# Kernel tuning notes

Measured on AMD Instinct MI355X. Metric: run time of the kernel, lower is better.

Reference implementation:

```python
import jax, jax.numpy as jnp
import numpy as np

N_SOTU, N_TAXON = 100000, 20000
E, EL = 800000, 200000
D_S, D_T, H = 256, 128, 256


def setup_inputs() -> dict:
    key = jax.random.key(0)
    ks = jax.random.split(key, 32)
    nrm = lambda k, shp: jax.random.normal(k, shp, jnp.float32) * 0.05
    inp = {}
    inp["x_sotu"] = nrm(ks[0], (N_SOTU, D_S))
    inp["x_taxon"] = nrm(ks[1], (N_TAXON, D_T))
    inp["edge_src"] = jax.random.randint(ks[2], (E,), 0, N_SOTU)   # sotu end
    inp["edge_dst"] = jax.random.randint(ks[3], (E,), 0, N_TAXON)  # taxon end
    inp["label_src"] = jax.random.randint(ks[4], (EL,), 0, N_SOTU)
    inp["label_dst"] = jax.random.randint(ks[5], (EL,), 0, N_TAXON)
    # conv1, edge type sotu->taxon
    inp["Wl1_st"] = nrm(ks[6], (H, D_S)); inp["bl1_st"] = jnp.zeros((H,), jnp.float32)
    inp["Wr1_st"] = nrm(ks[7], (H, D_T))
    # conv1, edge type taxon->sotu (reverse)
    inp["Wl1_ts"] = nrm(ks[8], (H, D_T)); inp["bl1_ts"] = jnp.zeros((H,), jnp.float32)
    inp["Wr1_ts"] = nrm(ks[9], (H, D_S))
    # conv2 (hidden -> hidden) per edge type
    inp["Wl2_st"] = nrm(ks[10], (H, H)); inp["bl2_st"] = jnp.zeros((H,), jnp.float32)
    inp["Wr2_st"] = nrm(ks[11], (H, H))
    inp["Wl2_ts"] = nrm(ks[12], (H, H)); inp["bl2_ts"] = jnp.zeros((H,), jnp.float32)
    inp["Wr2_ts"] = nrm(ks[13], (H, H))
    # final per-node-type linear (to_hetero duplicates Linear per node type)
    inp["Wlin_s"] = nrm(ks[14], (H, H)); inp["blin_s"] = jnp.zeros((H,), jnp.float32)
    inp["Wlin_t"] = nrm(ks[15], (H, H)); inp["blin_t"] = jnp.zeros((H,), jnp.float32)
    # edge decoder MLP
    inp["Wd1"] = nrm(ks[16], (H, 2 * H)); inp["bd1"] = jnp.zeros((H,), jnp.float32)
    inp["Wd2"] = nrm(ks[17], (1, H));     inp["bd2"] = jnp.zeros((1,), jnp.float32)
    return inp


def _sage(x_src, x_dst, src, dst, Wl, bl, Wr):
    """PyG SAGEConv (mean aggr): lin_l(mean of neighbor src feats) + lin_r(x_dst)."""
    n_dst = x_dst.shape[0]
    msum = jax.ops.segment_sum(x_src[src], dst, num_segments=n_dst)
    cnt = jax.ops.segment_sum(jnp.ones(src.shape, x_src.dtype), dst, num_segments=n_dst)
    m = msum / jnp.maximum(cnt, 1.0)[:, None]
    return m @ Wl.T + bl + x_dst @ Wr.T


def reference(x_sotu, x_taxon, edge_src, edge_dst, label_src, label_dst,
              Wl1_st, bl1_st, Wr1_st, Wl1_ts, bl1_ts, Wr1_ts,
              Wl2_st, bl2_st, Wr2_st, Wl2_ts, bl2_ts, Wr2_ts,
              Wlin_s, blin_s, Wlin_t, blin_t, Wd1, bd1, Wd2, bd2):
    # layer 1 (hetero SAGE, aggr='sum' over single incoming edge type per node type)
    h1_t = jax.nn.relu(_sage(x_sotu, x_taxon, edge_src, edge_dst, Wl1_st, bl1_st, Wr1_st))
    h1_s = jax.nn.relu(_sage(x_taxon, x_sotu, edge_dst, edge_src, Wl1_ts, bl1_ts, Wr1_ts))
    # layer 2
    h2_t = jax.nn.relu(_sage(h1_s, h1_t, edge_src, edge_dst, Wl2_st, bl2_st, Wr2_st))
    h2_s = jax.nn.relu(_sage(h1_t, h1_s, edge_dst, edge_src, Wl2_ts, bl2_ts, Wr2_ts))
    # per-node-type output projection
    z_s = h2_s @ Wlin_s.T + blin_s
    z_t = h2_t @ Wlin_t.T + blin_t
    # edge decoder: gather endpoint embeddings, concat, 2-layer MLP
    z = jnp.concatenate([z_s[label_src], z_t[label_dst]], axis=-1)  # [EL, 2H]
    h = jax.nn.relu(z @ Wd1.T + bd1)
    return (h @ Wd2.T + bd2).reshape(-1)  # [EL]
```

## Files before the change

### kernel.cpp

```cpp
#include <hip/hip_runtime.h>


constexpr int NS = 100000, NT = 20000;
constexpr int E_EDGES = 800000, EL_EDGES = 200000;
constexpr int DS = 256, DT = 128, H = 256;

constexpr int NB_T = 79, SH_T = 8, VB_T = 17;
constexpr int NB_S = 98, SH_S = 10, VB_S = 15;
constexpr int BIN_CAP = 96, CHUNK = 2048;
constexpr int CVT_BLOCKS = 2048;

typedef __attribute__((ext_vector_type(8))) short short8;
typedef __attribute__((ext_vector_type(4))) float float4v;
typedef __attribute__((ext_vector_type(8))) _Float16 half8v;
typedef unsigned short ushort_t;

__device__ __forceinline__ float bf2f(unsigned int u) {
    union { unsigned int i; float f; } x; x.i = u << 16; return x.f;
}
__device__ __forceinline__ unsigned short f2bf(float f) {
    union { float f; unsigned int i; } x; x.f = f;
    unsigned int r = x.i + 0x7FFFu + ((x.i >> 16) & 1u);
    return (unsigned short)(r >> 16);
}


struct GemmJob {
    const ushort_t* A1; const ushort_t* W1; int K1;
    const ushort_t* A2; const ushort_t* W2; int K2;
    const ushort_t* Add; const float* bias;
    void* C; int M; int flags;
};

struct GatherJob {
    const ushort_t* X; const int* rowptr; const int* cnt; const int* col;
    ushort_t* out; int N;
};

__device__ __forceinline__ void gemm_body(const GemmJob& jb, int bid)
{
    __shared__ ushort_t As[128][40];
    __shared__ ushort_t Bs[128][40];
    const int tid = threadIdx.x;
    const int M = jb.M;

    const int nx = (M + 127) >> 7;
    const int nx8 = nx & ~7;
    int rowblk, colblk;
    if (bid < nx8 * 2) {
        const int group = bid >> 4;
        const int xcd = bid & 7;
        const int half = (bid >> 3) & 1;
        rowblk = group * 8 + xcd;
        colblk = half;
    } else {
        const int r = bid - nx8 * 2;
        rowblk = nx8 + (r >> 1);
        colblk = r & 1;
    }
    const int row0 = rowblk * 128, col0 = colblk * 128;

    const int wave = tid >> 6, lane = tid & 63;
    const int wrow = (wave >> 1) * 32;
    const int wcol = (wave & 1) * 64;
    const int m16 = lane & 15, quad = lane >> 4;
    const int sr = tid >> 2;
    const int skc = (tid & 3) * 8;

    float4v acc[2][4];
#pragma unroll
    for (int i = 0; i < 2; i++)
#pragma unroll
        for (int j = 0; j < 4; j++) acc[i][j] = (float4v){0.f, 0.f, 0.f, 0.f};

#pragma unroll 1
    for (int pass = 0; pass < 2; pass++) {
        const ushort_t* A = pass ? jb.A2 : jb.A1;
        const ushort_t* W = pass ? jb.W2 : jb.W1;
        const int K = pass ? jb.K2 : jb.K1;
        if (!A) break;
        const int gra = row0 + sr;
        const bool oka = gra < M;
        const ushort_t* Ap = A + (size_t)gra * K + skc;
        const ushort_t* Wp = W + (size_t)(col0 + sr) * K + skc;

        uint4 a0 = make_uint4(0, 0, 0, 0);
        if (oka) a0 = *(const uint4*)Ap;
        uint4 b0 = *(const uint4*)Wp;

        for (int k0 = 0; k0 < K; k0 += 32) {
            __syncthreads();
            *(uint4*)&As[sr][skc] = a0;
            *(uint4*)&Bs[sr][skc] = b0;
            __syncthreads();
            if (k0 + 32 < K) {
                a0 = make_uint4(0, 0, 0, 0);
                if (oka) a0 = *(const uint4*)(Ap + k0 + 32);
                b0 = *(const uint4*)(Wp + k0 + 32);
            }
            short8 af[2], bf[4];
#pragma unroll
            for (int i = 0; i < 2; i++)
                af[i] = *(const short8*)&As[wrow + i * 16 + m16][quad * 8];
#pragma unroll
            for (int j = 0; j < 4; j++)
                bf[j] = *(const short8*)&Bs[wcol + j * 16 + m16][quad * 8];
#pragma unroll
            for (int i = 0; i < 2; i++)
#pragma unroll
                for (int j = 0; j < 4; j++)
                    acc[i][j] = __builtin_amdgcn_mfma_f32_16x16x32_bf16(
                        af[i], bf[j], acc[i][j], 0, 0, 0);
        }
    }

    const bool relu = jb.flags & 1, f16out = jb.flags & 2;
#pragma unroll
    for (int i = 0; i < 2; i++) {
        const int rbase = row0 + wrow + i * 16 + quad * 4;
#pragma unroll
        for (int r = 0; r < 4; r++) {
            const int row = rbase + r;
            if (row >= M) continue;
#pragma unroll
            for (int j = 0; j < 4; j++) {
                const int col = col0 + wcol + j * 16 + m16;
                float v = acc[i][j][r];
                if (jb.Add) v += bf2f((unsigned int)jb.Add[(size_t)row * 256 + col]);
                if (jb.bias) v += jb.bias[col];
                if (relu) v = fmaxf(v, 0.f);
                if (f16out) ((_Float16*)jb.C)[(size_t)row * 256 + col] = (_Float16)v;
                else ((ushort_t*)jb.C)[(size_t)row * 256 + col] = f2bf(v);
            }
        }
    }
}

__device__ __forceinline__ void gather_body(const GatherJob& g, int gb)
{
    const int node = gb * 16 + (threadIdx.x >> 5);
    const int c = (threadIdx.x & 31) * 8;
    if (node >= g.N) return;
    const int beg = g.rowptr[node];
    const int deg = g.cnt[node];
    const int end = beg + deg;
    const ushort_t* __restrict__ X = g.X;
    const int* __restrict__ col = g.col;
    float a[8] = {0, 0, 0, 0, 0, 0, 0, 0};
    float b[8] = {0, 0, 0, 0, 0, 0, 0, 0};
    int i = beg;
    for (; i + 1 < end; i += 2) {
        uint4 v = *(const uint4*)&X[(size_t)col[i] * 256 + c];
        uint4 w = *(const uint4*)&X[(size_t)col[i + 1] * 256 + c];
        a[0] += bf2f(v.x & 0xffff); a[1] += bf2f(v.x >> 16);
        a[2] += bf2f(v.y & 0xffff); a[3] += bf2f(v.y >> 16);
        a[4] += bf2f(v.z & 0xffff); a[5] += bf2f(v.z >> 16);
        a[6] += bf2f(v.w & 0xffff); a[7] += bf2f(v.w >> 16);
        b[0] += bf2f(w.x & 0xffff); b[1] += bf2f(w.x >> 16);
        b[2] += bf2f(w.y & 0xffff); b[3] += bf2f(w.y >> 16);
        b[4] += bf2f(w.z & 0xffff); b[5] += bf2f(w.z >> 16);
        b[6] += bf2f(w.w & 0xffff); b[7] += bf2f(w.w >> 16);
    }
    if (i < end) {
        uint4 v = *(const uint4*)&X[(size_t)col[i] * 256 + c];
        a[0] += bf2f(v.x & 0xffff); a[1] += bf2f(v.x >> 16);
        a[2] += bf2f(v.y & 0xffff); a[3] += bf2f(v.y >> 16);
        a[4] += bf2f(v.z & 0xffff); a[5] += bf2f(v.z >> 16);
        a[6] += bf2f(v.w & 0xffff); a[7] += bf2f(v.w >> 16);
    }
    float inv = 1.f / fmaxf((float)deg, 1.f);
    uint4 o;
    o.x = (unsigned int)f2bf((a[0] + b[0]) * inv) | ((unsigned int)f2bf((a[1] + b[1]) * inv) << 16);
    o.y = (unsigned int)f2bf((a[2] + b[2]) * inv) | ((unsigned int)f2bf((a[3] + b[3]) * inv) << 16);
    o.z = (unsigned int)f2bf((a[4] + b[4]) * inv) | ((unsigned int)f2bf((a[5] + b[5]) * inv) << 16);
    o.w = (unsigned int)f2bf((a[6] + b[6]) * inv) | ((unsigned int)f2bf((a[7] + b[7]) * inv) << 16);
    *(uint4*)&g.out[(size_t)node * 256 + c] = o;
}

__global__ __launch_bounds__(512) void mgemm_kernel(GemmJob a)
{
    gemm_body(a, blockIdx.x);
}

__global__ __launch_bounds__(512) void gemm_gather_kernel(GemmJob a, int ablocks,
                                                          GatherJob g)
{
    const int bid = blockIdx.x;
    if (bid < ablocks) gemm_body(a, bid);
    else gather_body(g, bid - ablocks);
}

__global__ __launch_bounds__(512) void gemm_gemm_kernel(GemmJob a, int ablocks,
                                                        GemmJob b)
{
    const int bid = blockIdx.x;
    if (bid < ablocks) gemm_body(a, bid);
    else gemm_body(b, bid - ablocks);
}

struct CvtJobs {
    const float* src[14];
    ushort_t* dst[14];
    int n4[14];
    int cnt;
};

__global__ __launch_bounds__(256) void cvt_kernel(CvtJobs jb, int nchunks)
{
    const int t = threadIdx.x;
#pragma unroll 1
    for (int ch = blockIdx.x; ch < nchunks; ch += gridDim.x) {
        int idx = ch << 10;
        int k = 0;
        while (idx >= jb.n4[k]) { idx -= jb.n4[k]; ++k; }
        const float4* __restrict__ s = (const float4*)jb.src[k];
        ushort_t* __restrict__ d = jb.dst[k];
        const int base = idx + t;
        float4 v0 = s[base];
        float4 v1 = s[base + 256];
        float4 v2 = s[base + 512];
        float4 v3 = s[base + 768];
        uint2 o0, o1, o2, o3;
        o0.x = (unsigned int)f2bf(v0.x) | ((unsigned int)f2bf(v0.y) << 16);
        o0.y = (unsigned int)f2bf(v0.z) | ((unsigned int)f2bf(v0.w) << 16);
        o1.x = (unsigned int)f2bf(v1.x) | ((unsigned int)f2bf(v1.y) << 16);
        o1.y = (unsigned int)f2bf(v1.z) | ((unsigned int)f2bf(v1.w) << 16);
        o2.x = (unsigned int)f2bf(v2.x) | ((unsigned int)f2bf(v2.y) << 16);
        o2.y = (unsigned int)f2bf(v2.z) | ((unsigned int)f2bf(v2.w) << 16);
        o3.x = (unsigned int)f2bf(v3.x) | ((unsigned int)f2bf(v3.y) << 16);
        o3.y = (unsigned int)f2bf(v3.z) | ((unsigned int)f2bf(v3.w) << 16);
        *(uint2*)(d + (size_t)base * 4) = o0;
        *(uint2*)(d + (size_t)(base + 256) * 4) = o1;
        *(uint2*)(d + (size_t)(base + 512) * 4) = o2;
        *(uint2*)(d + (size_t)(base + 768) * 4) = o3;
    }
}

__global__ __launch_bounds__(256) void count_kernel(
    const int* __restrict__ src, const int* __restrict__ dst,
    int* __restrict__ cnt_s, int* __restrict__ cnt_t, int E)
{
    const int base = blockIdx.x * 1024 + threadIdx.x;
    const int e0 = base, e1 = base + 256, e2 = base + 512, e3 = base + 768;
    int s0 = 0, s1 = 0, s2 = 0, s3 = 0;
    int d0 = 0, d1 = 0, d2 = 0, d3 = 0;
    if (e0 < E) { s0 = src[e0]; d0 = dst[e0]; }
    if (e1 < E) { s1 = src[e1]; d1 = dst[e1]; }
    if (e2 < E) { s2 = src[e2]; d2 = dst[e2]; }
    if (e3 < E) { s3 = src[e3]; d3 = dst[e3]; }
    if (e0 < E) { atomicAdd(&cnt_s[s0], 1); atomicAdd(&cnt_t[d0], 1); }
    if (e1 < E) { atomicAdd(&cnt_s[s1], 1); atomicAdd(&cnt_t[d1], 1); }
    if (e2 < E) { atomicAdd(&cnt_s[s2], 1); atomicAdd(&cnt_t[d2], 1); }
    if (e3 < E) { atomicAdd(&cnt_s[s3], 1); atomicAdd(&cnt_t[d3], 1); }
}

__global__ __launch_bounds__(256) void fold_kernel(
    const float* __restrict__ Wd1, const float* __restrict__ bd1,
    const float* __restrict__ Wlin_s, const float* __restrict__ blin_s,
    const float* __restrict__ Wlin_t, const float* __restrict__ blin_t,
    float* __restrict__ Wc_s, float* __restrict__ Wc_t,
    float* __restrict__ bu, float* __restrict__ bv)
{
    const int b = blockIdx.x, t = threadIdx.x;
    if (b < 256) {
        float s = 0.f;
        for (int k = 0; k < 256; k++) s += Wd1[b * 512 + k] * Wlin_s[k * 256 + t];
        Wc_s[b * 256 + t] = s;
    } else if (b < 512) {
        const int h = b - 256;
        float s = 0.f;
        for (int k = 0; k < 256; k++) s += Wd1[h * 512 + 256 + k] * Wlin_t[k * 256 + t];
        Wc_t[h * 256 + t] = s;
    } else {
        float su = 0.f, sv = 0.f;
        for (int k = 0; k < 256; k++) {
            su += Wd1[t * 512 + k] * blin_s[k];
            sv += Wd1[t * 512 + 256 + k] * blin_t[k];
        }
        bu[t] = bd1[t] + su;
        bv[t] = sv;
    }
}

__global__ __launch_bounds__(256) void psum_kernel(
    const int* __restrict__ cnt_s, const int* __restrict__ cnt_t,
    int* __restrict__ bsum_s, int* __restrict__ bsum_t, int nbS)
{
    const bool isS = (int)blockIdx.x < nbS;
    const int blk = isS ? blockIdx.x : blockIdx.x - nbS;
    const int N = isS ? NS : NT;
    const int* cnt = isS ? cnt_s : cnt_t;
    int* bsum = isS ? bsum_s : bsum_t;
    __shared__ int sdata[256];
    const int t = threadIdx.x;
    const int base = blk * 1024;
    int s = 0;
    for (int i = t; i < 1024; i += 256) {
        int idx = base + i;
        s += (idx < N) ? cnt[idx] : 0;
    }
    sdata[t] = s; __syncthreads();
    for (int off = 128; off > 0; off >>= 1) {
        if (t < off) sdata[t] += sdata[t + off];
        __syncthreads();
    }
    if (t == 0) bsum[blk] = sdata[0];
}

__global__ void sbsum_kernel(int* __restrict__ bsum_s, int* __restrict__ bsum_t,
                             int nbS, int nbT)
{
    if (threadIdx.x != 0) return;
    int* b = blockIdx.x ? bsum_t : bsum_s;
    int nb = blockIdx.x ? nbT : nbS;
    int run = 0;
    for (int i = 0; i < nb; i++) { int v = b[i]; b[i] = run; run += v; }
}

__global__ __launch_bounds__(256) void sblock_kernel(
    const int* __restrict__ cnt_s, const int* __restrict__ cnt_t,
    const int* __restrict__ bsum_s, const int* __restrict__ bsum_t,
    int* __restrict__ rowptr_s, int* __restrict__ rowptr_t, int nbS)
{
    const bool isS = (int)blockIdx.x < nbS;
    const int blk = isS ? blockIdx.x : blockIdx.x - nbS;
    const int N = isS ? NS : NT;
    const int* cnt = isS ? cnt_s : cnt_t;
    const int* bsum = isS ? bsum_s : bsum_t;
    int* rowptr = isS ? rowptr_s : rowptr_t;
    __shared__ int sc[256];
    const int t = threadIdx.x;
    const int base = blk * 1024 + t * 4;
    int v[4]; int s = 0;
#pragma unroll
    for (int j = 0; j < 4; j++) {
        int idx = base + j;
        v[j] = (idx < N) ? cnt[idx] : 0;
        s += v[j];
    }
    sc[t] = s; __syncthreads();
    for (int off = 1; off < 256; off <<= 1) {
        int add = (t >= off) ? sc[t - off] : 0;
        __syncthreads();
        sc[t] += add;
        __syncthreads();
    }
    int excl = sc[t] - s + bsum[blk];
#pragma unroll
    for (int j = 0; j < 4; j++) {
        int idx = base + j;
        if (idx < N) rowptr[idx] = excl;
        if (idx == N - 1) rowptr[N] = excl + v[j];
        excl += v[j];
    }
}

__global__ void binit_kernel(const int* __restrict__ rowptr_t,
                             const int* __restrict__ rowptr_s,
                             int* __restrict__ gcur_t, int* __restrict__ gcur_s)
{
    int t = threadIdx.x;
    if (t < NB_T) gcur_t[t] = rowptr_t[t << SH_T];
    if (t < NB_S) gcur_s[t] = rowptr_s[t << SH_S];
}

__global__ __launch_bounds__(256) void binA_kernel(
    const int* __restrict__ key, const int* __restrict__ val, int E,
    int nbins, int shift, int vbits,
    int* __restrict__ gcur, unsigned* __restrict__ stg)
{
    __shared__ unsigned bins[NB_S * BIN_CAP];
    __shared__ int lcnt[NB_S], gbase[NB_S];
    const int tid = threadIdx.x;
    const int base = blockIdx.x * CHUNK;
    for (int i = tid; i < nbins; i += 256) lcnt[i] = 0;
    __syncthreads();
    const unsigned lowmask = (1u << shift) - 1u;
#pragma unroll
    for (int k = 0; k < CHUNK / 256; k++) {
        int e = base + k * 256 + tid;
        if (e < E) {
            int kk = key[e];
            int b = kk >> shift;
            unsigned pk = (((unsigned)kk & lowmask) << vbits) | (unsigned)val[e];
            int c = atomicAdd(&lcnt[b], 1);
            if (c < BIN_CAP) bins[b * BIN_CAP + c] = pk;
            else { int p = atomicAdd(&gcur[b], 1); stg[p] = pk; }
        }
    }
    __syncthreads();
    if (tid < nbins) gbase[tid] = atomicAdd(&gcur[tid], min(lcnt[tid], BIN_CAP));
    __syncthreads();
    for (int b = 0; b < nbins; b++) {
        int c = min(lcnt[b], BIN_CAP);
        for (int i = tid; i < c; i += 256) stg[gbase[b] + i] = bins[b * BIN_CAP + i];
    }
}

__global__ __launch_bounds__(256) void binB_kernel(
    const unsigned* __restrict__ stg, const int* __restrict__ rowptr,
    int N, int node_per, int vbits, int* __restrict__ colout)
{
    __shared__ int cur[1024];
    const int tid = threadIdx.x;
    const int node0 = blockIdx.x * node_per;
    const int nn = min(node_per, N - node0);
    for (int i = tid; i < nn; i += 256) cur[i] = rowptr[node0 + i];
    const int estart = rowptr[node0];
    const int eend = rowptr[node0 + nn];
    __syncthreads();
    const unsigned vmask = (1u << vbits) - 1u;
    for (int i = estart + tid; i < eend; i += 256) {
        unsigned v = stg[i];
        int kl = (int)(v >> vbits);
        int pos = atomicAdd(&cur[kl], 1);
        colout[pos] = (int)(v & vmask);
    }
}

__global__ __launch_bounds__(256) void edge_score_kernel(
    const _Float16* __restrict__ U, const _Float16* __restrict__ V,
    const int* __restrict__ ls, const int* __restrict__ ld,
    const float* __restrict__ Wd2, const float* __restrict__ bd2,
    float* __restrict__ out, int EL)
{
    const int l32 = threadIdx.x & 31;
    const int e = blockIdx.x * 8 + (threadIdx.x >> 5);
    if (e >= EL) return;
    const int c = l32 * 8;
    half8v u = *(const half8v*)&U[(size_t)ls[e] * 256 + c];
    half8v v = *(const half8v*)&V[(size_t)ld[e] * 256 + c];
    float4 w0 = *(const float4*)&Wd2[c];
    float4 w1 = *(const float4*)&Wd2[c + 4];
    float s = fmaxf((float)u[0] + (float)v[0], 0.f) * w0.x
            + fmaxf((float)u[1] + (float)v[1], 0.f) * w0.y
            + fmaxf((float)u[2] + (float)v[2], 0.f) * w0.z
            + fmaxf((float)u[3] + (float)v[3], 0.f) * w0.w
            + fmaxf((float)u[4] + (float)v[4], 0.f) * w1.x
            + fmaxf((float)u[5] + (float)v[5], 0.f) * w1.y
            + fmaxf((float)u[6] + (float)v[6], 0.f) * w1.z
            + fmaxf((float)u[7] + (float)v[7], 0.f) * w1.w;
#pragma unroll
    for (int m = 16; m >= 1; m >>= 1) s += __shfl_xor(s, m, 64);
    if (l32 == 0) out[e] = s + bd2[0];
}

extern "C" void kernel_launch(void* const* d_in, const int* in_sizes, int n_in,
                              void* d_out, int out_size, void* d_ws, size_t ws_size,
                              hipStream_t stream)
{
    const float* x_sotu  = (const float*)d_in[0];
    const float* x_taxon = (const float*)d_in[1];
    const int* edge_src  = (const int*)d_in[2];
    const int* edge_dst  = (const int*)d_in[3];
    const int* label_src = (const int*)d_in[4];
    const int* label_dst = (const int*)d_in[5];
    const float* Wl1_st = (const float*)d_in[6];
    const float* bl1_st = (const float*)d_in[7];
    const float* Wr1_st = (const float*)d_in[8];
    const float* Wl1_ts = (const float*)d_in[9];
    const float* bl1_ts = (const float*)d_in[10];
    const float* Wr1_ts = (const float*)d_in[11];
    const float* Wl2_st = (const float*)d_in[12];
    const float* bl2_st = (const float*)d_in[13];
    const float* Wr2_st = (const float*)d_in[14];
    const float* Wl2_ts = (const float*)d_in[15];
    const float* bl2_ts = (const float*)d_in[16];
    const float* Wr2_ts = (const float*)d_in[17];
    const float* Wlin_s = (const float*)d_in[18];
    const float* blin_s = (const float*)d_in[19];
    const float* Wlin_t = (const float*)d_in[20];
    const float* blin_t = (const float*)d_in[21];
    const float* Wd1 = (const float*)d_in[22];
    const float* bd1 = (const float*)d_in[23];
    const float* Wd2 = (const float*)d_in[24];
    const float* bd2 = (const float*)d_in[25];

    int* wi = (int*)d_ws;
    size_t io = 0;
    int* cnt_s   = wi + io; io += NS;
    int* cnt_t   = wi + io; io += NT;
    int* rowptr_s = wi + io; io += NS + 8;
    int* rowptr_t = wi + io; io += NT + 8;
    int* col_s   = wi + io; io += E_EDGES;
    int* col_t   = wi + io; io += E_EDGES;
    unsigned* stg_s = (unsigned*)(wi + io); io += E_EDGES;
    unsigned* stg_t = (unsigned*)(wi + io); io += E_EDGES;
    int* bsum_s  = wi + io; io += 128;
    int* bsum_t  = wi + io; io += 128;
    int* gcur_t  = wi + io; io += 128;
    int* gcur_s  = wi + io; io += 128;
    io = (io + 63) & ~(size_t)63;

    ushort_t* wb = (ushort_t*)(wi + io);
    size_t bo = 0;
    ushort_t* m_s  = wb + bo; bo += (size_t)NS * H;
    ushort_t* h1_s = wb + bo; bo += (size_t)NS * H;
    ushort_t* m_t  = wb + bo; bo += (size_t)NT * H;
    ushort_t* h1_t = wb + bo; bo += (size_t)NT * H;
    ushort_t* h2_s = wb + bo; bo += (size_t)NS * H;
    ushort_t* h2_t = wb + bo; bo += (size_t)NT * H;
    ushort_t* xs_b = wb + bo; bo += (size_t)NS * DS;
    ushort_t* xt_b = wb + bo; bo += (size_t)NT * DT;
    ushort_t* Pt   = wb + bo; bo += (size_t)NT * H;
    ushort_t* wb_l1st = wb + bo; bo += H * DS;
    ushort_t* wb_r1st = wb + bo; bo += H * DT;
    ushort_t* wb_l1ts = wb + bo; bo += H * DT;
    ushort_t* wb_r1ts = wb + bo; bo += H * DS;
    ushort_t* wb_l2st = wb + bo; bo += H * H;
    ushort_t* wb_r2st = wb + bo; bo += H * H;
    ushort_t* wb_l2ts = wb + bo; bo += H * H;
    ushort_t* wb_r2ts = wb + bo; bo += H * H;
    ushort_t* wcb_s   = wb + bo; bo += H * H;
    ushort_t* wcb_t   = wb + bo; bo += H * H;
    bo = (bo + 7) & ~(size_t)7;

    float* wf = (float*)(wb + bo);
    size_t fo = 0;
    float* Wc_s = wf + fo; fo += H * H;
    float* Wc_t = wf + fo; fo += H * H;
    float* bu   = wf + fo; fo += 256;
    float* bv   = wf + fo; fo += 256;

    _Float16* U = (_Float16*)m_s;
    _Float16* V = (_Float16*)m_t;

    const dim3 blk(256);
    const dim3 blk512(512);
    auto mgn = [](int M) { return ((M + 127) / 128) * 2; };
    auto ggn = [](int N) { return (N + 15) / 16; };
    const int nbS = (NS + 1023) / 1024;
    const int nbT = (NT + 1023) / 1024;
    const int nA = (E_EDGES + CHUNK - 1) / CHUNK;

    fold_kernel<<<513, blk, 0, stream>>>(Wd1, bd1, Wlin_s, blin_s, Wlin_t, blin_t,
                                         Wc_s, Wc_t, bu, bv);

    hipMemsetAsync(cnt_s, 0, (size_t)(NS + NT) * sizeof(int), stream);
    count_kernel<<<(E_EDGES + 1023) / 1024, blk, 0, stream>>>(
        edge_src, edge_dst, cnt_s, cnt_t, E_EDGES);

    {
        CvtJobs jb; int c = 0, total4 = 0;
        auto addj = [&](const float* s, ushort_t* d, int n) {
            jb.src[c] = s; jb.dst[c] = d; jb.n4[c] = n / 4; total4 += n / 4; c++;
        };
        addj(x_sotu, xs_b, NS * DS);
        addj(x_taxon, xt_b, NT * DT);
        addj(Wl1_st, wb_l1st, H * DS);
        addj(Wr1_st, wb_r1st, H * DT);
        addj(Wl1_ts, wb_l1ts, H * DT);
        addj(Wr1_ts, wb_r1ts, H * DS);
        addj(Wl2_st, wb_l2st, H * H);
        addj(Wr2_st, wb_r2st, H * H);
        addj(Wl2_ts, wb_l2ts, H * H);
        addj(Wr2_ts, wb_r2ts, H * H);
        addj(Wc_s, wcb_s, H * H);
        addj(Wc_t, wcb_t, H * H);
        jb.cnt = c;
        const int nchunks = total4 >> 10;
        const int cvb = nchunks < CVT_BLOCKS ? nchunks : CVT_BLOCKS;
        cvt_kernel<<<cvb, blk, 0, stream>>>(jb, nchunks);
    }

    psum_kernel<<<nbS + nbT, blk, 0, stream>>>(cnt_s, cnt_t, bsum_s, bsum_t, nbS);
    sbsum_kernel<<<2, 64, 0, stream>>>(bsum_s, bsum_t, nbS, nbT);
    sblock_kernel<<<nbS + nbT, blk, 0, stream>>>(cnt_s, cnt_t, bsum_s, bsum_t,
                                                 rowptr_s, rowptr_t, nbS);
    binit_kernel<<<1, blk, 0, stream>>>(rowptr_t, rowptr_s, gcur_t, gcur_s);
    binA_kernel<<<nA, blk, 0, stream>>>(edge_dst, edge_src, E_EDGES,
                                        NB_T, SH_T, VB_T, gcur_t, stg_t);
    binA_kernel<<<nA, blk, 0, stream>>>(edge_src, edge_dst, E_EDGES,
                                        NB_S, SH_S, VB_S, gcur_s, stg_s);
    binB_kernel<<<NB_T, blk, 0, stream>>>(stg_t, rowptr_t, NT, 1 << SH_T, VB_T, col_t);
    binB_kernel<<<NB_S, blk, 0, stream>>>(stg_s, rowptr_s, NS, 1 << SH_S, VB_S, col_s);

    {
        GemmJob a{xt_b, wb_l1ts, DT, nullptr, nullptr, 0, nullptr, nullptr, Pt, NT, 0};
        GatherJob g{xs_b, rowptr_t, cnt_t, col_t, m_t, NT};
        const int ab = mgn(NT);
        gemm_gather_kernel<<<ab + ggn(NT), blk512, 0, stream>>>(a, ab, g);
    }
    {
        GemmJob a{m_t, wb_l1st, H, xt_b, wb_r1st, DT, nullptr, bl1_st, h1_t, NT, 1};
        GatherJob g{Pt, rowptr_s, cnt_s, col_s, m_s, NS};
        const int ab = mgn(NT);
        gemm_gather_kernel<<<ab + ggn(NS), blk512, 0, stream>>>(a, ab, g);
    }
    {
        GemmJob a{xs_b, wb_r1ts, DS, nullptr, nullptr, 0, m_s, bl1_ts, h1_s, NS, 1};
        mgemm_kernel<<<mgn(NS), blk512, 0, stream>>>(a);
    }

    {
        GemmJob a{h1_t, wb_l2ts, H, nullptr, nullptr, 0, nullptr, nullptr, Pt, NT, 0};
        GatherJob g{h1_s, rowptr_t, cnt_t, col_t, m_t, NT};
        const int ab = mgn(NT);
        gemm_gather_kernel<<<ab + ggn(NT), blk512, 0, stream>>>(a, ab, g);
    }
    {
        GemmJob a{m_t, wb_l2st, H, h1_t, wb_r2st, H, nullptr, bl2_st, h2_t, NT, 1};
        GatherJob g{Pt, rowptr_s, cnt_s, col_s, m_s, NS};
        const int ab = mgn(NT);
        gemm_gather_kernel<<<ab + ggn(NS), blk512, 0, stream>>>(a, ab, g);
    }
    {
        GemmJob a{h1_s, wb_r2ts, H, nullptr, nullptr, 0, m_s, bl2_ts, h2_s, NS, 1};
        mgemm_kernel<<<mgn(NS), blk512, 0, stream>>>(a);
    }

    {
        GemmJob a{h2_s, wcb_s, H, nullptr, nullptr, 0, nullptr, bu, U, NS, 2};
        GemmJob b{h2_t, wcb_t, H, nullptr, nullptr, 0, nullptr, bv, V, NT, 2};
        const int ab = mgn(NS);
        gemm_gemm_kernel<<<ab + mgn(NT), blk512, 0, stream>>>(a, ab, b);
    }
    edge_score_kernel<<<(EL_EDGES + 7) / 8, blk, 0, stream>>>(
        U, V, label_src, label_dst, Wd2, bd2, (float*)d_out, EL_EDGES);
}
```

Baseline: 926.4 us.

## Aggregate before projecting on sotu side and pair gathers and GEMMs per layer

The sotu-side SAGE aggregation now gathers raw neighbor features and folds the lin_l projection into a dual-operand GEMM, instead of projecting taxon features first and then gathering the projected rows. Layer 1 adds a 128-wide gather variant so the sotu-side gather reads half-width rows. Each layer becomes one fused gather kernel (both directions) followed by one fused dual GEMM kernel (both node types), removing the Pt intermediate and cutting launch count. The trade-off is extra GEMM work on the 100k-row sotu side (an added K segment), in exchange for less random gather traffic in layer 1 and fewer, larger launches.

```diff
diff --git a/kernel.cpp b/kernel.cpp
--- a/kernel.cpp
+++ b/kernel.cpp
@@ -33,6 +33,11 @@
 };
 
 struct GatherJob {
+    const ushort_t* X; const int* rowptr; const int* cnt; const int* col;
+    ushort_t* out; int N;
+};
+
+struct Gather128Job {
     const ushort_t* X; const int* rowptr; const int* cnt; const int* col;
     ushort_t* out; int N;
 };
@@ -177,17 +182,45 @@
     *(uint4*)&g.out[(size_t)node * 256 + c] = o;
 }
 
-__global__ __launch_bounds__(512) void mgemm_kernel(GemmJob a)
-{
-    gemm_body(a, blockIdx.x);
-}
-
-__global__ __launch_bounds__(512) void gemm_gather_kernel(GemmJob a, int ablocks,
-                                                          GatherJob g)
-{
-    const int bid = blockIdx.x;
-    if (bid < ablocks) gemm_body(a, bid);
-    else gather_body(g, bid - ablocks);
+__device__ __forceinline__ void gather128_body(const Gather128Job& g, int gb)
+{
+    const int node = gb * 32 + (threadIdx.x >> 4);
+    const int c = (threadIdx.x & 15) * 8;
+    if (node >= g.N) return;
+    const int beg = g.rowptr[node];
+    const int deg = g.cnt[node];
+    const int end = beg + deg;
+    const ushort_t* __restrict__ X = g.X;
+    const int* __restrict__ col = g.col;
+    float a[8] = {0, 0, 0, 0, 0, 0, 0, 0};
+    float b[8] = {0, 0, 0, 0, 0, 0, 0, 0};
+    int i = beg;
+    for (; i + 1 < end; i += 2) {
+        uint4 v = *(const uint4*)&X[(size_t)col[i] * 128 + c];
+        uint4 w = *(const uint4*)&X[(size_t)col[i + 1] * 128 + c];
+        a[0] += bf2f(v.x & 0xffff); a[1] += bf2f(v.x >> 16);
+        a[2] += bf2f(v.y & 0xffff); a[3] += bf2f(v.y >> 16);
+        a[4] += bf2f(v.z & 0xffff); a[5] += bf2f(v.z >> 16);
+        a[6] += bf2f(v.w & 0xffff); a[7] += bf2f(v.w >> 16);
+        b[0] += bf2f(w.x & 0xffff); b[1] += bf2f(w.x >> 16);
+        b[2] += bf2f(w.y & 0xffff); b[3] += bf2f(w.y >> 16);
+        b[4] += bf2f(w.z & 0xffff); b[5] += bf2f(w.z >> 16);
+        b[6] += bf2f(w.w & 0xffff); b[7] += bf2f(w.w >> 16);
+    }
+    if (i < end) {
+        uint4 v = *(const uint4*)&X[(size_t)col[i] * 128 + c];
+        a[0] += bf2f(v.x & 0xffff); a[1] += bf2f(v.x >> 16);
+        a[2] += bf2f(v.y & 0xffff); a[3] += bf2f(v.y >> 16);
+        a[4] += bf2f(v.z & 0xffff); a[5] += bf2f(v.z >> 16);
+        a[6] += bf2f(v.w & 0xffff); a[7] += bf2f(v.w >> 16);
+    }
+    float inv = 1.f / fmaxf((float)deg, 1.f);
+    uint4 o;
+    o.x = (unsigned int)f2bf((a[0] + b[0]) * inv) | ((unsigned int)f2bf((a[1] + b[1]) * inv) << 16);
+    o.y = (unsigned int)f2bf((a[2] + b[2]) * inv) | ((unsigned int)f2bf((a[3] + b[3]) * inv) << 16);
+    o.z = (unsigned int)f2bf((a[4] + b[4]) * inv) | ((unsigned int)f2bf((a[5] + b[5]) * inv) << 16);
+    o.w = (unsigned int)f2bf((a[6] + b[6]) * inv) | ((unsigned int)f2bf((a[7] + b[7]) * inv) << 16);
+    *(uint4*)&g.out[(size_t)node * 128 + c] = o;
 }
 
 __global__ __launch_bounds__(512) void gemm_gemm_kernel(GemmJob a, int ablocks,
@@ -196,6 +229,22 @@
     const int bid = blockIdx.x;
     if (bid < ablocks) gemm_body(a, bid);
     else gemm_body(b, bid - ablocks);
+}
+
+__global__ __launch_bounds__(512) void gather_g128_kernel(GatherJob a, int ablocks,
+                                                          Gather128Job b)
+{
+    const int bid = blockIdx.x;
+    if (bid < ablocks) gather_body(a, bid);
+    else gather128_body(b, bid - ablocks);
+}
+
+__global__ __launch_bounds__(512) void gather_gather_kernel(GatherJob a, int ablocks,
+                                                            GatherJob b)
+{
+    const int bid = blockIdx.x;
+    if (bid < ablocks) gather_body(a, bid);
+    else gather_body(b, bid - ablocks);
 }
 
 struct CvtJobs {
@@ -502,7 +551,6 @@
     ushort_t* h2_t = wb + bo; bo += (size_t)NT * H;
     ushort_t* xs_b = wb + bo; bo += (size_t)NS * DS;
     ushort_t* xt_b = wb + bo; bo += (size_t)NT * DT;
-    ushort_t* Pt   = wb + bo; bo += (size_t)NT * H;
     ushort_t* wb_l1st = wb + bo; bo += H * DS;
     ushort_t* wb_r1st = wb + bo; bo += H * DT;
     ushort_t* wb_l1ts = wb + bo; bo += H * DT;
@@ -528,7 +576,8 @@
     const dim3 blk(256);
     const dim3 blk512(512);
     auto mgn = [](int M) { return ((M + 127) / 128) * 2; };
-    auto ggn = [](int N) { return (N + 15) / 16; };
+    auto g256n = [](int N) { return (N + 15) / 16; };
+    auto g128n = [](int N) { return (N + 31) / 32; };
     const int nbS = (NS + 1023) / 1024;
     const int nbT = (NT + 1023) / 1024;
     const int nA = (E_EDGES + CHUNK - 1) / CHUNK;
@@ -576,37 +625,29 @@
     binB_kernel<<<NB_S, blk, 0, stream>>>(stg_s, rowptr_s, NS, 1 << SH_S, VB_S, col_s);
 
     {
-        GemmJob a{xt_b, wb_l1ts, DT, nullptr, nullptr, 0, nullptr, nullptr, Pt, NT, 0};
-        GatherJob g{xs_b, rowptr_t, cnt_t, col_t, m_t, NT};
-        const int ab = mgn(NT);
-        gemm_gather_kernel<<<ab + ggn(NT), blk512, 0, stream>>>(a, ab, g);
+        GatherJob a{xs_b, rowptr_t, cnt_t, col_t, m_t, NT};
+        Gather128Job b{xt_b, rowptr_s, cnt_s, col_s, m_s, NS};
+        const int ab = g256n(NT);
+        gather_g128_kernel<<<ab + g128n(NS), blk512, 0, stream>>>(a, ab, b);
     }
     {
-        GemmJob a{m_t, wb_l1st, H, xt_b, wb_r1st, DT, nullptr, bl1_st, h1_t, NT, 1};
-        GatherJob g{Pt, rowptr_s, cnt_s, col_s, m_s, NS};
-        const int ab = mgn(NT);
-        gemm_gather_kernel<<<ab + ggn(NS), blk512, 0, stream>>>(a, ab, g);
-    }
+        GemmJob a{xs_b, wb_r1ts, DS, m_s, wb_l1ts, DT, nullptr, bl1_ts, h1_s, NS, 1};
+        GemmJob b{m_t, wb_l1st, H, xt_b, wb_r1st, DT, nullptr, bl1_st, h1_t, NT, 1};
+        const int ab = mgn(NS);
+        gemm_gemm_kernel<<<ab + mgn(NT), blk512, 0, stream>>>(a, ab, b);
+    }
+
     {
-        GemmJob a{xs_b, wb_r1ts, DS, nullptr, nullptr, 0, m_s, bl1_ts, h1_s, NS, 1};
-        mgemm_kernel<<<mgn(NS), blk512, 0, stream>>>(a);
-    }
-
+        GatherJob a{h1_s, rowptr_t, cnt_t, col_t, m_t, NT};
+        GatherJob b{h1_t, rowptr_s, cnt_s, col_s, m_s, NS};
+        const int ab = g256n(NT);
+        gather_gather_kernel<<<ab + g256n(NS), blk512, 0, stream>>>(a, ab, b);
+    }
     {
-        GemmJob a{h1_t, wb_l2ts, H, nullptr, nullptr, 0, nullptr, nullptr, Pt, NT, 0};
-        GatherJob g{h1_s, rowptr_t, cnt_t, col_t, m_t, NT};
-        const int ab = mgn(NT);
-        gemm_gather_kernel<<<ab + ggn(NT), blk512, 0, stream>>>(a, ab, g);
-    }
-    {
-        GemmJob a{m_t, wb_l2st, H, h1_t, wb_r2st, H, nullptr, bl2_st, h2_t, NT, 1};
-        GatherJob g{Pt, rowptr_s, cnt_s, col_s, m_s, NS};
-        const int ab = mgn(NT);
-        gemm_gather_kernel<<<ab + ggn(NS), blk512, 0, stream>>>(a, ab, g);
-    }
-    {
-        GemmJob a{h1_s, wb_r2ts, H, nullptr, nullptr, 0, m_s, bl2_ts, h2_s, NS, 1};
-        mgemm_kernel<<<mgn(NS), blk512, 0, stream>>>(a);
+        GemmJob a{h1_s, wb_r2ts, H, m_s, wb_l2ts, H, nullptr, bl2_ts, h2_s, NS, 1};
+        GemmJob b{m_t, wb_l2st, H, h1_t, wb_r2st, H, nullptr, bl2_st, h2_t, NT, 1};
+        const int ab = mgn(NS);
+        gemm_gemm_kernel<<<ab + mgn(NT), blk512, 0, stream>>>(a, ab, b);
     }
 
     {
```

Result: faster. 795.0 us (-14.2%).
